# Optimization experiments

Measured on AMD Instinct MI355X. Metric: run time of the kernel, lower is better.

Reference implementation:

```python
import jax, jax.numpy as jnp
import numpy as np

B, C, T, H = 1024, 64, 1024, 32


def setup_inputs() -> dict:
    key = jax.random.key(0)
    k1, k2, k3, k4, k5 = jax.random.split(key, 5)
    s = 1.0 / np.sqrt(H)  # PyTorch GRU init scale
    return {
        "x": jax.random.normal(k1, (B, C, T), dtype=jnp.float32),
        "W_ih": jax.random.uniform(k2, (3 * H, C), dtype=jnp.float32, minval=-s, maxval=s),
        "W_hh": jax.random.uniform(k3, (3 * H, H), dtype=jnp.float32, minval=-s, maxval=s),
        "b_ih": jax.random.uniform(k4, (3 * H,), dtype=jnp.float32, minval=-s, maxval=s),
        "b_hh": jax.random.uniform(k5, (3 * H,), dtype=jnp.float32, minval=-s, maxval=s),
    }


def _gru_last_hidden(x, W_ih, W_hh, b_ih, b_hh):
    # x: [B, C, T] -> [B, T, C] (mirrors x.permute(0, 2, 1))
    xt = jnp.transpose(x, (0, 2, 1))
    h = W_hh.shape[1]
    # Precompute input-to-hidden projections for all timesteps: [B, T, 3H]
    gx = jnp.einsum('btc,gc->btg', xt, W_ih) + b_ih
    gx = jnp.swapaxes(gx, 0, 1)  # [T, B, 3H] for scan over time
    h0 = jnp.zeros((x.shape[0], h), dtype=x.dtype)

    def step(h_prev, gx_t):
        gh = h_prev @ W_hh.T + b_hh  # [B, 3H]
        xr, xz, xn = gx_t[:, :h], gx_t[:, h:2 * h], gx_t[:, 2 * h:]
        hr, hz, hn = gh[:, :h], gh[:, h:2 * h], gh[:, 2 * h:]
        r = jax.nn.sigmoid(xr + hr)
        z = jax.nn.sigmoid(xz + hz)
        n = jnp.tanh(xn + r * hn)
        h_new = (1.0 - z) * n + z * h_prev
        return h_new, None

    h_last, _ = jax.lax.scan(step, h0, gx)
    return h_last  # [B, H] == embed[:, -1]


def reference(x, W_ih, W_hh, b_ih, b_hh):
    return _gru_last_hidden(x, W_ih, W_hh, b_ih, b_hh)
```

## Files before the change

kernel.cpp:

```cpp
#include <hip/hip_runtime.h>


typedef short bf16x8 __attribute__((ext_vector_type(8)));
typedef float f32x4  __attribute__((ext_vector_type(4)));
typedef float f32x2  __attribute__((ext_vector_type(2)));

#define TT 32
#define GXS 97
#define LDS_BYTES 157056
#define NLOG2E -1.44269504088896340736f
#define P2LOG2E 2.88539008177792681472f

#define GLL16(gp, lp)                                                        \
  __builtin_amdgcn_global_load_lds(                                          \
      (const __attribute__((address_space(1))) void*)(gp),                   \
      (__attribute__((address_space(3))) void*)(lp), 16, 0, 0)

static __device__ __forceinline__ short f2bf(float f) {
    unsigned u = __float_as_uint(f);
    u += 0x7fffu + ((u >> 16) & 1u);
    return (short)(u >> 16);
}
static __device__ __forceinline__ float bf2f(short s) {
    return __uint_as_float(((unsigned)(unsigned short)s) << 16);
}

__global__ __launch_bounds__(512) void gru_fused18(
    const float* __restrict__ x,
    const float* __restrict__ W_ih,
    const float* __restrict__ W_hh,
    const float* __restrict__ b_ih,
    const float* __restrict__ b_hh,
    float* __restrict__ out)
{
    extern __shared__ char smem[];
    short* wfH   = (short*)smem;
    short* wfL   = (short*)(smem + 12288);
    float* xs    = (float*)(smem + 24576);
    float* gxs   = (float*)(smem + 57344);
    float* biasc = (float*)(smem + 156672);

    const int tid  = threadIdx.x;
    const int wid  = tid >> 6;
    const int lane = tid & 63;
    const int bid  = blockIdx.x;

    for (int f = tid; f < 768; f += 512) {
        int slot = f & 63, ktnt = f >> 6;
        int kt = ktnt / 6, nt = ktnt - kt * 6;
        int g  = nt * 16 + (slot & 15);
        int c0 = kt * 32 + (slot >> 4) * 8;
        const float sc = (g < 64) ? NLOG2E : P2LOG2E;
        const float* wr = W_ih + g * 64 + c0;
        bf16x8 hi, lo;
        #pragma unroll
        for (int j = 0; j < 8; ++j) {
            float v  = wr[j] * sc;
            short hb = f2bf(v);
            hi[j] = hb;
            lo[j] = f2bf(v - bf2f(hb));
        }
        *(bf16x8*)(wfH + f * 8) = hi;
        *(bf16x8*)(wfL + f * 8) = lo;
    }
    if (tid < 96) {
        const float sc = (tid < 64) ? NLOG2E : P2LOG2E;
        biasc[tid] = (b_ih[tid] + (tid < 64 ? b_hh[tid] : 0.f)) * sc;
    }

    const float* xb = nullptr;
    if (wid < 4) xb = x + (size_t)(bid * 4 + wid) * 64 * 1024;

    const int h  = lane & 31;
    const int h3 = h * 3;
    f32x2 wg2[16], wn2[16];
    float bhn = 0.f, hout = 0.f;
    if (wid >= 4) {
        const int grow = (lane < 32) ? h : (32 + h);
        #pragma unroll
        for (int j = 0; j < 16; ++j) {
            f32x2 a = *(const f32x2*)(W_hh + grow * 32 + 2 * j);
            f32x2 b = *(const f32x2*)(W_hh + (64 + h) * 32 + 2 * j);
            wg2[j].x = a.x * NLOG2E;  wg2[j].y = a.y * NLOG2E;
            wn2[j].x = b.x * P2LOG2E; wn2[j].y = b.y * P2LOG2E;
        }
        bhn = b_hh[64 + h] * P2LOG2E;
    }

    auto load_xtile = [&](int tile) {
        const int tbase = tile * TT;
        const int c_lo  = lane >> 3;
        #pragma unroll
        for (int i = 0; i < 8; ++i) {
            const int toff = (((lane & 7) << 2) ^ ((i & 3) << 3));
            const float* gp = xb + (i * 8 + c_lo) * 1024 + tbase + toff;
            float* lp = xs + wid * 2048 + i * 256;
            GLL16(gp, lp);
        }
    };

    auto stage1 = [&](int buf, int prefetch_tile) {
        float* gb = gxs + buf * 12416 + wid * 3104;
        #pragma unroll
        for (int mt = 0; mt < 2; ++mt) {
            bf16x8 ah[2], al[2];
            const int tS = (mt * 16 + (lane & 15)) ^ ((lane >> 4) << 3);
            #pragma unroll
            for (int kt = 0; kt < 2; ++kt) {
                const int cb = kt * 32 + (lane >> 4) * 8;
                float xf[8];
                #pragma unroll
                for (int j = 0; j < 8; ++j)
                    xf[j] = xs[wid * 2048 + (cb + j) * 32 + tS];
                #pragma unroll
                for (int j = 0; j < 8; ++j) {
                    short hb_ = f2bf(xf[j]);
                    ah[kt][j] = hb_;
                    al[kt][j] = f2bf(xf[j] - bf2f(hb_));
                }
            }
            const int row0 = mt * 16 + ((lane >> 4) << 2);
            #pragma unroll
            for (int nt = 0; nt < 6; ++nt) {
                const int g   = nt * 16 + (lane & 15);
                const int off = (g & 31) * 3 + (g >> 5);
                const float bias = biasc[g];
                f32x4 acc = {bias, bias, bias, bias};
                bf16x8 b0 = *(const bf16x8*)(wfH + ((nt)     * 64 + lane) * 8);
                bf16x8 b1 = *(const bf16x8*)(wfH + ((6 + nt) * 64 + lane) * 8);
                acc = __builtin_amdgcn_mfma_f32_16x16x32_bf16(ah[0], b0, acc, 0, 0, 0);
                acc = __builtin_amdgcn_mfma_f32_16x16x32_bf16(ah[1], b1, acc, 0, 0, 0);
                acc = __builtin_amdgcn_mfma_f32_16x16x32_bf16(al[0], b0, acc, 0, 0, 0);
                acc = __builtin_amdgcn_mfma_f32_16x16x32_bf16(al[1], b1, acc, 0, 0, 0);
                b0 = *(const bf16x8*)(wfL + ((nt)     * 64 + lane) * 8);
                b1 = *(const bf16x8*)(wfL + ((6 + nt) * 64 + lane) * 8);
                acc = __builtin_amdgcn_mfma_f32_16x16x32_bf16(ah[0], b0, acc, 0, 0, 0);
                acc = __builtin_amdgcn_mfma_f32_16x16x32_bf16(ah[1], b1, acc, 0, 0, 0);
                #pragma unroll
                for (int j = 0; j < 4; ++j)
                    gb[(row0 + j) * GXS + off] = acc[j];
            }
            if (mt == 0) __builtin_amdgcn_sched_barrier(0);
        }
        asm volatile("s_waitcnt lgkmcnt(0)" ::: "memory");
        if (prefetch_tile >= 0) load_xtile(prefetch_tile);
    };

    auto stage2 = [&](int buf) {
        const float* gb = gxs + buf * 12416 + (wid - 4) * 3104 + h3;
        __builtin_amdgcn_s_setprio(1);
        float xr0 = gb[0],       xz0 = gb[1],       xn0 = gb[2];
        float xr1 = gb[GXS],     xz1 = gb[GXS + 1], xn1 = gb[GXS + 2];
        #pragma unroll
        for (int s = 0; s < TT; ++s) {
            float xr2 = 0.f, xz2 = 0.f, xn2 = 0.f;
            if (s < TT - 2) {
                const float* nrow = gb + (s + 2) * GXS;
                xr2 = nrow[0]; xz2 = nrow[1]; xn2 = nrow[2];
            }
            f32x2 aA0 = {0.f, 0.f}, aA1 = {0.f, 0.f};
            f32x2 aN0 = {0.f, 0.f}, aN1 = {0.f, 0.f};
            const int hb = __float_as_int(hout);
            #pragma unroll
            for (int j = 0; j < 16; j += 2) {
                float s0 = __int_as_float(__builtin_amdgcn_readlane(hb, 2 * j));
                float s1 = __int_as_float(__builtin_amdgcn_readlane(hb, 2 * j + 1));
                float s2 = __int_as_float(__builtin_amdgcn_readlane(hb, 2 * j + 2));
                float s3 = __int_as_float(__builtin_amdgcn_readlane(hb, 2 * j + 3));
                f32x2 h01 = {s0, s1}, h23 = {s2, s3};
                aA0 = __builtin_elementwise_fma(wg2[j],     h01, aA0);
                aA1 = __builtin_elementwise_fma(wg2[j + 1], h23, aA1);
                aN0 = __builtin_elementwise_fma(wn2[j],     h01, aN0);
                aN1 = __builtin_elementwise_fma(wn2[j + 1], h23, aN1);
            }
            f32x2 aA = aA0 + aA1;
            f32x2 aN = aN0 + aN1;
            float accA = aA.x + aA.y;
            float swA = accA, swB = accA;
            asm volatile("v_permlane32_swap_b32 %0, %1"
                         : "+v"(swA), "+v"(swB));
            float accO = (swA + swB) - accA;
            float accN = aN.x + aN.y;
            float accR = (lane < 32) ? accA : accO;
            float accZ = (lane < 32) ? accO : accA;
            float r = __builtin_amdgcn_rcpf(
                          1.f + __builtin_amdgcn_exp2f(xr0 + accR));
            float z = __builtin_amdgcn_rcpf(
                          1.f + __builtin_amdgcn_exp2f(xz0 + accZ));
            float u  = fmaf(r, accN + bhn, xn0);
            float n  = fmaf(-2.f, __builtin_amdgcn_rcpf(
                                      __builtin_amdgcn_exp2f(u) + 1.f), 1.f);
            hout = n + z * (hout - n);
            xr0 = xr1; xz0 = xz1; xn0 = xn1;
            xr1 = xr2; xz1 = xz2; xn1 = xn2;
        }
        __builtin_amdgcn_s_setprio(0);
    };

    if (wid < 4) load_xtile(0);
    __syncthreads();

    if (wid < 4) stage1(0, 1);
    __syncthreads();

    for (int k = 0; k < 32; ++k) {
        if (wid >= 4) {
            stage2(k & 1);
        } else if (k < 31) {
            stage1((k + 1) & 1, (k < 30) ? (k + 2) : -1);
        }
        __syncthreads();
    }

    if (wid >= 4 && lane < 32)
        out[(bid * 4 + (wid - 4)) * 32 + h] = hout;
}

extern "C" void kernel_launch(void* const* d_in, const int* in_sizes, int n_in,
                              void* d_out, int out_size, void* d_ws, size_t ws_size,
                              hipStream_t stream) {
    const float* x    = (const float*)d_in[0];
    const float* W_ih = (const float*)d_in[1];
    const float* W_hh = (const float*)d_in[2];
    const float* b_ih = (const float*)d_in[3];
    const float* b_hh = (const float*)d_in[4];
    float* out = (float*)d_out;

    hipFuncSetAttribute((const void*)gru_fused18,
                        hipFuncAttributeMaxDynamicSharedMemorySize, LDS_BYTES);
    gru_fused18<<<256, 512, LDS_BYTES, stream>>>(x, W_ih, W_hh, b_ih, b_hh, out);
}
```

Before: 233.5 us.

## Use fp16 dot2 for recurrent matvec and compute one sigmoid per lane

The hidden-state matvec in the serial recurrence now packs pairs of h values into fp16 (the second value comes from a DPP row-rotate) and uses v_dot2 instructions. This halves the readlane broadcasts and FMA count on the critical sequential path. Each lane also evaluates only its own gate sigmoid (r or z) and swaps the result across wave halves, instead of swapping pre-activations and computing both sigmoids. The cost is fp16 rounding of weights and hidden state, which may reduce accuracy across 1024 recurrent steps. The weight pairing also depends on a runtime probe of the DPP rotate direction.

```diff
diff --git a/kernel.cpp b/kernel.cpp
--- a/kernel.cpp
+++ b/kernel.cpp
@@ -4,6 +4,8 @@
 typedef short bf16x8 __attribute__((ext_vector_type(8)));
 typedef float f32x4  __attribute__((ext_vector_type(4)));
 typedef float f32x2  __attribute__((ext_vector_type(2)));
+typedef _Float16 f16x2 __attribute__((ext_vector_type(2)));
+typedef __fp16 fp16v2 __attribute__((ext_vector_type(2)));
 
 #define TT 32
 #define GXS 97
@@ -11,6 +13,12 @@
 #define NLOG2E -1.44269504088896340736f
 #define P2LOG2E 2.88539008177792681472f
 
+#if __has_builtin(__builtin_amdgcn_fdot2)
+#define HAVE_DOT2 1
+#else
+#define HAVE_DOT2 0
+#endif
+
 #define GLL16(gp, lp)                                                        \
   __builtin_amdgcn_global_load_lds(                                          \
       (const __attribute__((address_space(1))) void*)(gp),                   \
@@ -24,8 +32,13 @@
 static __device__ __forceinline__ float bf2f(short s) {
     return __uint_as_float(((unsigned)(unsigned short)s) << 16);
 }
-
-__global__ __launch_bounds__(512) void gru_fused18(
+static __device__ __forceinline__ float ror1(float x) {
+    return __int_as_float(__builtin_amdgcn_update_dpp(
+        0, __float_as_int(x), 0x121, 0xf, 0xf, true));
+}
+union HPk { int i; f16x2 h; fp16v2 p; };
+
+__global__ __launch_bounds__(512) void gru_fused20(
     const float* __restrict__ x,
     const float* __restrict__ W_ih,
     const float* __restrict__ W_hh,
@@ -73,8 +86,31 @@
 
     const int h  = lane & 31;
     const int h3 = h * 3;
+    float bhn = 0.f, hout = 0.f;
+
+    const float rotF = ror1((float)(lane & 15));
+    const bool dirPlus =
+        (__builtin_amdgcn_readlane(__float_as_int(rotF), 0) ==
+         __float_as_int(1.0f));
+
+#if HAVE_DOT2
+    f16x2 wgp[16], wnp[16];
+    if (wid >= 4) {
+        const int grow = (lane < 32) ? h : (32 + h);
+        #pragma unroll
+        for (int j = 0; j < 16; ++j) {
+            const int ke = 2 * j;
+            const int ko = dirPlus ? (ke + 1)
+                                   : ((ke & 16) | ((ke + 15) & 15));
+            wgp[j][0] = (_Float16)(W_hh[grow * 32 + ke] * NLOG2E);
+            wgp[j][1] = (_Float16)(W_hh[grow * 32 + ko] * NLOG2E);
+            wnp[j][0] = (_Float16)(W_hh[(64 + h) * 32 + ke] * P2LOG2E);
+            wnp[j][1] = (_Float16)(W_hh[(64 + h) * 32 + ko] * P2LOG2E);
+        }
+        bhn = b_hh[64 + h] * P2LOG2E;
+    }
+#else
     f32x2 wg2[16], wn2[16];
-    float bhn = 0.f, hout = 0.f;
     if (wid >= 4) {
         const int grow = (lane < 32) ? h : (32 + h);
         #pragma unroll
@@ -86,6 +122,7 @@
         }
         bhn = b_hh[64 + h] * P2LOG2E;
     }
+#endif
 
     auto load_xtile = [&](int tile) {
         const int tbase = tile * TT;
@@ -148,18 +185,35 @@
 
     auto stage2 = [&](int buf) {
         const float* gb = gxs + buf * 12416 + (wid - 4) * 3104 + h3;
+        const int sel = (lane >> 5) & 1;
         __builtin_amdgcn_s_setprio(1);
-        float xr0 = gb[0],       xz0 = gb[1],       xn0 = gb[2];
-        float xr1 = gb[GXS],     xz1 = gb[GXS + 1], xn1 = gb[GXS + 2];
+        float xg0 = gb[sel],       xn0 = gb[2];
+        float xg1 = gb[GXS + sel], xn1 = gb[GXS + 2];
         #pragma unroll
         for (int s = 0; s < TT; ++s) {
-            float xr2 = 0.f, xz2 = 0.f, xn2 = 0.f;
+            float xg2 = 0.f, xn2 = 0.f;
             if (s < TT - 2) {
-                const float* nrow = gb + (s + 2) * GXS;
-                xr2 = nrow[0]; xz2 = nrow[1]; xn2 = nrow[2];
-            }
-            f32x2 aA0 = {0.f, 0.f}, aA1 = {0.f, 0.f};
-            f32x2 aN0 = {0.f, 0.f}, aN1 = {0.f, 0.f};
+                xg2 = gb[(s + 2) * GXS + sel];
+                xn2 = gb[(s + 2) * GXS + 2];
+            }
+            float aA0 = 0.f, aA1 = 0.f, aN0 = 0.f, aN1 = 0.f;
+#if HAVE_DOT2
+            HPk hp; hp.p = __builtin_amdgcn_cvt_pkrtz(hout, ror1(hout));
+            const int hpb = hp.i;
+            #pragma unroll
+            for (int j = 0; j < 16; j += 2) {
+                HPk p0; p0.i = __builtin_amdgcn_readlane(hpb, 2 * j);
+                HPk p1; p1.i = __builtin_amdgcn_readlane(hpb, 2 * j + 2);
+                aA0 = __builtin_amdgcn_fdot2(wgp[j],     p0.h, aA0, false);
+                aA1 = __builtin_amdgcn_fdot2(wgp[j + 1], p1.h, aA1, false);
+                aN0 = __builtin_amdgcn_fdot2(wnp[j],     p0.h, aN0, false);
+                aN1 = __builtin_amdgcn_fdot2(wnp[j + 1], p1.h, aN1, false);
+            }
+            float accA = aA0 + aA1;
+            float accN = aN0 + aN1;
+#else
+            f32x2 vA0 = {0.f, 0.f}, vA1 = {0.f, 0.f};
+            f32x2 vN0 = {0.f, 0.f}, vN1 = {0.f, 0.f};
             const int hb = __float_as_int(hout);
             #pragma unroll
             for (int j = 0; j < 16; j += 2) {
@@ -168,31 +222,29 @@
                 float s2 = __int_as_float(__builtin_amdgcn_readlane(hb, 2 * j + 2));
                 float s3 = __int_as_float(__builtin_amdgcn_readlane(hb, 2 * j + 3));
                 f32x2 h01 = {s0, s1}, h23 = {s2, s3};
-                aA0 = __builtin_elementwise_fma(wg2[j],     h01, aA0);
-                aA1 = __builtin_elementwise_fma(wg2[j + 1], h23, aA1);
-                aN0 = __builtin_elementwise_fma(wn2[j],     h01, aN0);
-                aN1 = __builtin_elementwise_fma(wn2[j + 1], h23, aN1);
-            }
-            f32x2 aA = aA0 + aA1;
-            f32x2 aN = aN0 + aN1;
-            float accA = aA.x + aA.y;
-            float swA = accA, swB = accA;
+                vA0 = __builtin_elementwise_fma(wg2[j],     h01, vA0);
+                vA1 = __builtin_elementwise_fma(wg2[j + 1], h23, vA1);
+                vN0 = __builtin_elementwise_fma(wn2[j],     h01, vN0);
+                vN1 = __builtin_elementwise_fma(wn2[j + 1], h23, vN1);
+            }
+            f32x2 vA = vA0 + vA1, vN = vN0 + vN1;
+            float accA = vA.x + vA.y;
+            float accN = vN.x + vN.y;
+#endif
+            float sig = __builtin_amdgcn_rcpf(
+                            1.f + __builtin_amdgcn_exp2f(xg0 + accA));
+            float swA = sig, swB = sig;
             asm volatile("v_permlane32_swap_b32 %0, %1"
                          : "+v"(swA), "+v"(swB));
-            float accO = (swA + swB) - accA;
-            float accN = aN.x + aN.y;
-            float accR = (lane < 32) ? accA : accO;
-            float accZ = (lane < 32) ? accO : accA;
-            float r = __builtin_amdgcn_rcpf(
-                          1.f + __builtin_amdgcn_exp2f(xr0 + accR));
-            float z = __builtin_amdgcn_rcpf(
-                          1.f + __builtin_amdgcn_exp2f(xz0 + accZ));
+            float oth = (swA + swB) - sig;
+            float r = (lane < 32) ? sig : oth;
+            float z = (lane < 32) ? oth : sig;
             float u  = fmaf(r, accN + bhn, xn0);
             float n  = fmaf(-2.f, __builtin_amdgcn_rcpf(
                                       __builtin_amdgcn_exp2f(u) + 1.f), 1.f);
             hout = n + z * (hout - n);
-            xr0 = xr1; xz0 = xz1; xn0 = xn1;
-            xr1 = xr2; xz1 = xz2; xn1 = xn2;
+            xg0 = xg1; xn0 = xn1;
+            xg1 = xg2; xn1 = xn2;
         }
         __builtin_amdgcn_s_setprio(0);
     };
@@ -226,7 +278,7 @@
     const float* b_hh = (const float*)d_in[4];
     float* out = (float*)d_out;
 
-    hipFuncSetAttribute((const void*)gru_fused18,
+    hipFuncSetAttribute((const void*)gru_fused20,
                         hipFuncAttributeMaxDynamicSharedMemorySize, LDS_BYTES);
-    gru_fused18<<<256, 512, LDS_BYTES, stream>>>(x, W_ih, W_hh, b_ih, b_hh, out);
-}
+    gru_fused20<<<256, 512, LDS_BYTES, stream>>>(x, W_ih, W_hh, b_ih, b_hh, out);
+}
```

Measured after the change: 191.7 us. 1.22x faster.
